# Performance work log

Hardware: AMD Instinct MI355X
Metric: run time of the kernel (lower is better)

## Reference

```python
import jax, jax.numpy as jnp
import numpy as np

N_NODES, N_EDGES, D_IN, D_OUT = 50000, 400000, 512, 512


def setup_inputs() -> dict:
    key = jax.random.key(0)
    k = jax.random.split(key, 7)
    s = 1.0 / np.sqrt(D_IN)
    return {
        "x": jax.random.normal(k[0], (N_NODES, D_IN), dtype=jnp.float32),
        "src": jax.random.randint(k[1], (N_EDGES,), 0, N_NODES),
        "dst": jax.random.randint(k[2], (N_EDGES,), 0, N_NODES),
        "W1": jax.random.uniform(k[3], (D_IN, D_OUT), jnp.float32, -s, s),
        "b1": jax.random.uniform(k[4], (D_OUT,), jnp.float32, -s, s),
        "W2": jax.random.uniform(k[5], (D_IN, D_OUT), jnp.float32, -s, s),
        "b2": jax.random.uniform(k[6], (D_OUT,), jnp.float32, -s, s),
    }


def reference(x, src, dst, W1, b1, W2, b2):
    n_nodes = x.shape[0]
    # gather src features along each edge, segment-sum into dst nodes
    msg_sum = jax.ops.segment_sum(x[src], dst, num_segments=n_nodes)      # [N, D_in]
    counts = jax.ops.segment_sum(jnp.ones_like(dst, dtype=x.dtype), dst,
                                 num_segments=n_nodes)                    # [N]
    mean = msg_sum / jnp.maximum(counts, 1.0)[:, None]                    # mailbox mean
    out = (x @ W1 + b1) + ((x - mean) @ W2 + b2)
    # DGL update_all leaves nodes with no incoming messages untouched
    return jnp.where((counts > 0)[:, None], out, x)
```

## Files before the change

kernel.cpp:

```cpp
#include <hip/hip_runtime.h>
#include <hip/hip_bf16.h>
#include <stdint.h>

typedef unsigned short u16;
typedef unsigned int   u32;

#define N_NODES 50000
#define N_EDGES 400000
#define DDIM    512

typedef __attribute__((ext_vector_type(8))) __bf16 bf16x8;
typedef __attribute__((ext_vector_type(4))) float  f32x4;

__device__ __forceinline__ float bflo(u32 d) { return __builtin_bit_cast(float, d << 16); }
__device__ __forceinline__ float bfhi(u32 d) { return __builtin_bit_cast(float, d & 0xffff0000u); }
__device__ __forceinline__ u16 f2bf(float f) {
    u32 u = __builtin_bit_cast(u32, f);
    u32 r = u + 0x7fffu + ((u >> 16) & 1u);
    return (u16)(r >> 16);
}
__device__ __forceinline__ u32 pack2(float a, float b) {
    return (u32)f2bf(a) | ((u32)f2bf(b) << 16);
}
__device__ __forceinline__ void gload_lds16(const void* g, void* l) {
    __builtin_amdgcn_global_load_lds(
        (const __attribute__((address_space(1))) void*)g,
        (__attribute__((address_space(3))) void*)l, 16, 0, 0);
}

__global__ void cvt_k(const float* __restrict__ x, u16* __restrict__ xb) {
    int i = blockIdx.x * 256 + threadIdx.x;
    const float4* p = (const float4*)(x + (size_t)i * 8);
    float4 a = p[0], b = p[1];
    uint4 o;
    o.x = pack2(a.x, a.y); o.y = pack2(a.z, a.w);
    o.z = pack2(b.x, b.y); o.w = pack2(b.z, b.w);
    ((uint4*)xb)[i] = o;
}

__global__ void hist_k(const int* __restrict__ dst, int* __restrict__ counts) {
    int e = blockIdx.x * 256 + threadIdx.x;
    if (e < N_EDGES) atomicAdd(&counts[dst[e]], 1);
}

#define NCHUNK 49
__global__ __launch_bounds__(1024) void scanA_k(const int* __restrict__ counts, int* __restrict__ csum) {
    __shared__ int ws[16];
    int t = threadIdx.x, b = blockIdx.x;
    int i = b * 1024 + t;
    int v = (i < N_NODES) ? counts[i] : 0;
    for (int d = 32; d; d >>= 1) v += __shfl_down(v, d);
    if ((t & 63) == 0) ws[t >> 6] = v;
    __syncthreads();
    if (t < 16) {
        int s = ws[t];
        for (int d = 8; d; d >>= 1) s += __shfl_down(s, d);
        if (t == 0) csum[b] = s;
    }
}
__global__ void scanB_k(int* __restrict__ csum) {
    int t = threadIdx.x;
    int v = (t < NCHUNK) ? csum[t] : 0;
    int s = v;
    for (int d = 1; d < 64; d <<= 1) { int u = __shfl_up(s, d); if (t >= d) s += u; }
    if (t < NCHUNK) csum[t] = s - v;
}
__global__ __launch_bounds__(1024) void scanC_k(const int* __restrict__ counts, const int* __restrict__ csum,
                                                int* __restrict__ offsets, int* __restrict__ cursor) {
    __shared__ int wsum[16];
    int t = threadIdx.x, b = blockIdx.x;
    int i = b * 1024 + t;
    int lane = t & 63, w = t >> 6;
    int v = (i < N_NODES) ? counts[i] : 0;
    int s = v;
    for (int d = 1; d < 64; d <<= 1) { int u = __shfl_up(s, d); if (lane >= d) s += u; }
    if (lane == 63) wsum[w] = s;
    __syncthreads();
    if (t < 16) {
        int ww = wsum[t], ss = ww;
        for (int d = 1; d < 16; d <<= 1) { int u = __shfl_up(ss, d); if (t >= d) ss += u; }
        wsum[t] = ss - ww;
    }
    __syncthreads();
    int excl = (s - v) + wsum[w] + csum[b];
    if (i < N_NODES) { offsets[i] = excl; cursor[i] = excl; }
}

__global__ void fill_k(const int* __restrict__ src, const int* __restrict__ dst,
                       int* __restrict__ cursor, int* __restrict__ esrc) {
    int e = blockIdx.x * 256 + threadIdx.x;
    if (e < N_EDGES) {
        int d = dst[e];
        int p = atomicAdd(&cursor[d], 1);
        esrc[p] = src[e];
    }
}

__global__ void prepw_k(const float* __restrict__ W1, const float* __restrict__ W2,
                        const float* __restrict__ b1, const float* __restrict__ b2,
                        u16* __restrict__ Wt12, u16* __restrict__ Wt2, float* __restrict__ b12) {
    int idx = blockIdx.x * 256 + threadIdx.x;
    int k = idx >> 9, n = idx & 511;
    float w1 = W1[idx], w2 = W2[idx];
    Wt12[n * 512 + k] = f2bf(w1 + w2);
    Wt2[n * 512 + k]  = f2bf(w2);
    if (idx < 512) b12[idx] = b1[idx] + b2[idx];
}

__device__ __forceinline__ void addrow(float* acc, uint4 v) {
    acc[0] += bflo(v.x); acc[1] += bfhi(v.x);
    acc[2] += bflo(v.y); acc[3] += bfhi(v.y);
    acc[4] += bflo(v.z); acc[5] += bfhi(v.z);
    acc[6] += bflo(v.w); acc[7] += bfhi(v.w);
}
__global__ __launch_bounds__(256) void agg_k(const u16* __restrict__ xb,
                                             const int* __restrict__ offsets,
                                             const int* __restrict__ counts,
                                             const int* __restrict__ esrc,
                                             u16* __restrict__ meanNeg) {
    int nid = blockIdx.x * 4 + (threadIdx.x >> 6);
    if (nid >= N_NODES) return;
    int lane = threadIdx.x & 63;
    int off = offsets[nid], deg = counts[nid];
    float acc[8] = {0, 0, 0, 0, 0, 0, 0, 0};
    int e = 0;
    for (; e + 3 < deg; e += 4) {
        int s0 = esrc[off + e], s1 = esrc[off + e + 1];
        int s2 = esrc[off + e + 2], s3 = esrc[off + e + 3];
        uint4 v0 = *(const uint4*)(xb + (size_t)s0 * DDIM + lane * 8);
        uint4 v1 = *(const uint4*)(xb + (size_t)s1 * DDIM + lane * 8);
        uint4 v2 = *(const uint4*)(xb + (size_t)s2 * DDIM + lane * 8);
        uint4 v3 = *(const uint4*)(xb + (size_t)s3 * DDIM + lane * 8);
        addrow(acc, v0); addrow(acc, v1); addrow(acc, v2); addrow(acc, v3);
    }
    for (; e < deg; e++) {
        int s0 = esrc[off + e];
        addrow(acc, *(const uint4*)(xb + (size_t)s0 * DDIM + lane * 8));
    }
    float scale = (deg > 0) ? (-1.0f / (float)deg) : 0.0f;
    uint4 o;
    o.x = pack2(acc[0] * scale, acc[1] * scale);
    o.y = pack2(acc[2] * scale, acc[3] * scale);
    o.z = pack2(acc[4] * scale, acc[5] * scale);
    o.w = pack2(acc[6] * scale, acc[7] * scale);
    *(uint4*)(meanNeg + (size_t)nid * DDIM + lane * 8) = o;
}

__global__ __launch_bounds__(256) void gemm_k(const u16* __restrict__ xb,
                                              const float* __restrict__ x,
                                              const u16* __restrict__ meanNeg,
                                              const u16* __restrict__ Wt12,
                                              const u16* __restrict__ Wt2,
                                              const float* __restrict__ b12,
                                              const int* __restrict__ counts,
                                              float* __restrict__ out) {
    __shared__ u16 As[128 * 32];
    __shared__ u16 Bs[128 * 32];
    const int m0 = blockIdx.x * 128;
    const int n0 = blockIdx.y * 128;
    const int tid = threadIdx.x;
    const int lane = tid & 63;
    const int wid  = tid >> 6;
    const int wm = wid >> 1, wn = wid & 1;
    const int quad = lane >> 4, lr = lane & 15;

    f32x4 acc[4][4] = {};

    const int skoff = (lane & 3) * 8;
    const int srsub = lane >> 2;
    int arow[2], brow[2];
    #pragma unroll
    for (int t = 0; t < 2; t++) {
        int r = wid * 32 + t * 16 + srsub;
        int ar = m0 + r; if (ar >= N_NODES) ar = N_NODES - 1;
        arow[t] = ar;
        brow[t] = n0 + r;
    }

    for (int pass = 0; pass < 2; pass++) {
        const u16* __restrict__ A = pass ? meanNeg : xb;
        const u16* __restrict__ B = pass ? Wt2 : Wt12;
        for (int k0 = 0; k0 < 512; k0 += 32) {
            #pragma unroll
            for (int t = 0; t < 2; t++) {
                int rblk = wid * 32 + t * 16;
                gload_lds16(A + (size_t)arow[t] * DDIM + k0 + skoff, &As[rblk * 32]);
                gload_lds16(B + (size_t)brow[t] * DDIM + k0 + skoff, &Bs[rblk * 32]);
            }
            __syncthreads();
            bf16x8 af[4], bfr[4];
            #pragma unroll
            for (int i = 0; i < 4; i++)
                af[i] = *(const bf16x8*)&As[(wm * 64 + i * 16 + lr) * 32 + quad * 8];
            #pragma unroll
            for (int j = 0; j < 4; j++)
                bfr[j] = *(const bf16x8*)&Bs[(wn * 64 + j * 16 + lr) * 32 + quad * 8];
            #pragma unroll
            for (int i = 0; i < 4; i++)
                #pragma unroll
                for (int j = 0; j < 4; j++)
                    acc[i][j] = __builtin_amdgcn_mfma_f32_16x16x32_bf16(af[i], bfr[j], acc[i][j], 0, 0, 0);
            __syncthreads();
        }
    }

    #pragma unroll
    for (int i = 0; i < 4; i++) {
        #pragma unroll
        for (int r = 0; r < 4; r++) {
            int grow = m0 + wm * 64 + i * 16 + quad * 4 + r;
            if (grow >= N_NODES) continue;
            int cnt = counts[grow];
            #pragma unroll
            for (int j = 0; j < 4; j++) {
                int gcol = n0 + wn * 64 + j * 16 + lr;
                float v;
                if (cnt > 0) v = acc[i][j][r] + b12[gcol];
                else         v = x[(size_t)grow * DDIM + gcol];
                out[(size_t)grow * DDIM + gcol] = v;
            }
        }
    }
}

extern "C" void kernel_launch(void* const* d_in, const int* in_sizes, int n_in,
                              void* d_out, int out_size, void* d_ws, size_t ws_size,
                              hipStream_t stream) {
    const float* x  = (const float*)d_in[0];
    const int* src  = (const int*)d_in[1];
    const int* dst  = (const int*)d_in[2];
    const float* W1 = (const float*)d_in[3];
    const float* b1 = (const float*)d_in[4];
    const float* W2 = (const float*)d_in[5];
    const float* b2 = (const float*)d_in[6];
    float* out = (float*)d_out;

    char* ws = (char*)d_ws;
    size_t o = 0;
    auto alloc = [&](size_t bytes) { char* p = ws + o; o += (bytes + 255) & ~(size_t)255; return p; };
    int* counts   = (int*)alloc((size_t)N_NODES * 4);
    int* offsets  = (int*)alloc((size_t)N_NODES * 4);
    int* cursor   = (int*)alloc((size_t)N_NODES * 4);
    int* csum     = (int*)alloc((size_t)NCHUNK * 4);
    int* esrc     = (int*)alloc((size_t)N_EDGES * 4);
    u16* Wt12     = (u16*)alloc((size_t)512 * 512 * 2);
    u16* Wt2      = (u16*)alloc((size_t)512 * 512 * 2);
    float* b12    = (float*)alloc((size_t)512 * 4);
    u16* xb       = (u16*)alloc((size_t)N_NODES * DDIM * 2);
    u16* meanNeg  = (u16*)alloc((size_t)N_NODES * DDIM * 2);
    (void)ws_size; (void)n_in; (void)in_sizes; (void)out_size;

    hipMemsetAsync(counts, 0, (size_t)N_NODES * 4, stream);
    cvt_k<<<(N_NODES * DDIM / 8) / 256, 256, 0, stream>>>(x, xb);
    hist_k<<<(N_EDGES + 255) / 256, 256, 0, stream>>>(dst, counts);
    scanA_k<<<NCHUNK, 1024, 0, stream>>>(counts, csum);
    scanB_k<<<1, 64, 0, stream>>>(csum);
    scanC_k<<<NCHUNK, 1024, 0, stream>>>(counts, csum, offsets, cursor);
    fill_k<<<(N_EDGES + 255) / 256, 256, 0, stream>>>(src, dst, cursor, esrc);
    prepw_k<<<(512 * 512) / 256, 256, 0, stream>>>(W1, W2, b1, b2, Wt12, Wt2, b12);
    agg_k<<<(N_NODES + 3) / 4, 256, 0, stream>>>(xb, offsets, counts, esrc, meanNeg);
    gemm_k<<<dim3((N_NODES + 127) / 128, DDIM / 128), 256, 0, stream>>>(
        xb, x, meanNeg, Wt12, Wt2, b12, counts, out);
}
```

Measured before the change: 433.9 us.

## Double GEMM K-tile, remap grid for L2 reuse, unroll aggregation by eight

The GEMM now stages 64-wide K tiles in LDS instead of 32, which halves the number of barrier pairs per pass. It also launches a 1D grid where the four N-tiles of one M-block are adjacent, so neighbouring blocks reuse the same A rows from L2. The aggregation kernel gains an 8-way unrolled gather loop to keep more row loads in flight. The trade-off is twice the LDS per block, which may reduce occupancy, plus higher register pressure in the aggregation kernel.

```diff
diff --git a/kernel.cpp b/kernel.cpp
--- a/kernel.cpp
+++ b/kernel.cpp
@@ -123,19 +123,36 @@
     int lane = threadIdx.x & 63;
     int off = offsets[nid], deg = counts[nid];
     float acc[8] = {0, 0, 0, 0, 0, 0, 0, 0};
+    const size_t lo = (size_t)lane * 8;
     int e = 0;
+    for (; e + 7 < deg; e += 8) {
+        int s0 = esrc[off + e],     s1 = esrc[off + e + 1];
+        int s2 = esrc[off + e + 2], s3 = esrc[off + e + 3];
+        int s4 = esrc[off + e + 4], s5 = esrc[off + e + 5];
+        int s6 = esrc[off + e + 6], s7 = esrc[off + e + 7];
+        uint4 v0 = *(const uint4*)(xb + (size_t)s0 * DDIM + lo);
+        uint4 v1 = *(const uint4*)(xb + (size_t)s1 * DDIM + lo);
+        uint4 v2 = *(const uint4*)(xb + (size_t)s2 * DDIM + lo);
+        uint4 v3 = *(const uint4*)(xb + (size_t)s3 * DDIM + lo);
+        uint4 v4 = *(const uint4*)(xb + (size_t)s4 * DDIM + lo);
+        uint4 v5 = *(const uint4*)(xb + (size_t)s5 * DDIM + lo);
+        uint4 v6 = *(const uint4*)(xb + (size_t)s6 * DDIM + lo);
+        uint4 v7 = *(const uint4*)(xb + (size_t)s7 * DDIM + lo);
+        addrow(acc, v0); addrow(acc, v1); addrow(acc, v2); addrow(acc, v3);
+        addrow(acc, v4); addrow(acc, v5); addrow(acc, v6); addrow(acc, v7);
+    }
     for (; e + 3 < deg; e += 4) {
-        int s0 = esrc[off + e], s1 = esrc[off + e + 1];
+        int s0 = esrc[off + e],     s1 = esrc[off + e + 1];
         int s2 = esrc[off + e + 2], s3 = esrc[off + e + 3];
-        uint4 v0 = *(const uint4*)(xb + (size_t)s0 * DDIM + lane * 8);
-        uint4 v1 = *(const uint4*)(xb + (size_t)s1 * DDIM + lane * 8);
-        uint4 v2 = *(const uint4*)(xb + (size_t)s2 * DDIM + lane * 8);
-        uint4 v3 = *(const uint4*)(xb + (size_t)s3 * DDIM + lane * 8);
+        uint4 v0 = *(const uint4*)(xb + (size_t)s0 * DDIM + lo);
+        uint4 v1 = *(const uint4*)(xb + (size_t)s1 * DDIM + lo);
+        uint4 v2 = *(const uint4*)(xb + (size_t)s2 * DDIM + lo);
+        uint4 v3 = *(const uint4*)(xb + (size_t)s3 * DDIM + lo);
         addrow(acc, v0); addrow(acc, v1); addrow(acc, v2); addrow(acc, v3);
     }
     for (; e < deg; e++) {
         int s0 = esrc[off + e];
-        addrow(acc, *(const uint4*)(xb + (size_t)s0 * DDIM + lane * 8));
+        addrow(acc, *(const uint4*)(xb + (size_t)s0 * DDIM + lo));
     }
     float scale = (deg > 0) ? (-1.0f / (float)deg) : 0.0f;
     uint4 o;
@@ -143,7 +160,7 @@
     o.y = pack2(acc[2] * scale, acc[3] * scale);
     o.z = pack2(acc[4] * scale, acc[5] * scale);
     o.w = pack2(acc[6] * scale, acc[7] * scale);
-    *(uint4*)(meanNeg + (size_t)nid * DDIM + lane * 8) = o;
+    *(uint4*)(meanNeg + (size_t)nid * DDIM + lo) = o;
 }
 
 __global__ __launch_bounds__(256) void gemm_k(const u16* __restrict__ xb,
@@ -154,10 +171,11 @@
                                               const float* __restrict__ b12,
                                               const int* __restrict__ counts,
                                               float* __restrict__ out) {
-    __shared__ u16 As[128 * 32];
-    __shared__ u16 Bs[128 * 32];
-    const int m0 = blockIdx.x * 128;
-    const int n0 = blockIdx.y * 128;
+    __shared__ u16 As[128 * 64];
+    __shared__ u16 Bs[128 * 64];
+    const int bid = blockIdx.x;
+    const int m0 = (bid >> 2) * 128;
+    const int n0 = (bid & 3) * 128;
     const int tid = threadIdx.x;
     const int lane = tid & 63;
     const int wid  = tid >> 6;
@@ -166,12 +184,11 @@
 
     f32x4 acc[4][4] = {};
 
-    const int skoff = (lane & 3) * 8;
-    const int srsub = lane >> 2;
-    int arow[2], brow[2];
+    const int kk = (lane & 7) * 8;
+    int arow[4], brow[4];
     #pragma unroll
-    for (int t = 0; t < 2; t++) {
-        int r = wid * 32 + t * 16 + srsub;
+    for (int t = 0; t < 4; t++) {
+        int r = wid * 32 + t * 8 + (lane >> 3);
         int ar = m0 + r; if (ar >= N_NODES) ar = N_NODES - 1;
         arow[t] = ar;
         brow[t] = n0 + r;
@@ -180,26 +197,29 @@
     for (int pass = 0; pass < 2; pass++) {
         const u16* __restrict__ A = pass ? meanNeg : xb;
         const u16* __restrict__ B = pass ? Wt2 : Wt12;
-        for (int k0 = 0; k0 < 512; k0 += 32) {
+        for (int k0 = 0; k0 < 512; k0 += 64) {
             #pragma unroll
-            for (int t = 0; t < 2; t++) {
-                int rblk = wid * 32 + t * 16;
-                gload_lds16(A + (size_t)arow[t] * DDIM + k0 + skoff, &As[rblk * 32]);
-                gload_lds16(B + (size_t)brow[t] * DDIM + k0 + skoff, &Bs[rblk * 32]);
+            for (int t = 0; t < 4; t++) {
+                int rblk = wid * 32 + t * 8;
+                gload_lds16(A + (size_t)arow[t] * DDIM + k0 + kk, &As[rblk * 64]);
+                gload_lds16(B + (size_t)brow[t] * DDIM + k0 + kk, &Bs[rblk * 64]);
             }
             __syncthreads();
-            bf16x8 af[4], bfr[4];
             #pragma unroll
-            for (int i = 0; i < 4; i++)
-                af[i] = *(const bf16x8*)&As[(wm * 64 + i * 16 + lr) * 32 + quad * 8];
-            #pragma unroll
-            for (int j = 0; j < 4; j++)
-                bfr[j] = *(const bf16x8*)&Bs[(wn * 64 + j * 16 + lr) * 32 + quad * 8];
-            #pragma unroll
-            for (int i = 0; i < 4; i++)
+            for (int ks = 0; ks < 2; ks++) {
+                bf16x8 af[4], bfr[4];
+                #pragma unroll
+                for (int i = 0; i < 4; i++)
+                    af[i] = *(const bf16x8*)&As[(wm * 64 + i * 16 + lr) * 64 + ks * 32 + quad * 8];
                 #pragma unroll
                 for (int j = 0; j < 4; j++)
-                    acc[i][j] = __builtin_amdgcn_mfma_f32_16x16x32_bf16(af[i], bfr[j], acc[i][j], 0, 0, 0);
+                    bfr[j] = *(const bf16x8*)&Bs[(wn * 64 + j * 16 + lr) * 64 + ks * 32 + quad * 8];
+                #pragma unroll
+                for (int i = 0; i < 4; i++)
+                    #pragma unroll
+                    for (int j = 0; j < 4; j++)
+                        acc[i][j] = __builtin_amdgcn_mfma_f32_16x16x32_bf16(af[i], bfr[j], acc[i][j], 0, 0, 0);
+            }
             __syncthreads();
         }
     }
@@ -259,6 +279,6 @@
     fill_k<<<(N_EDGES + 255) / 256, 256, 0, stream>>>(src, dst, cursor, esrc);
     prepw_k<<<(512 * 512) / 256, 256, 0, stream>>>(W1, W2, b1, b2, Wt12, Wt2, b12);
     agg_k<<<(N_NODES + 3) / 4, 256, 0, stream>>>(xb, offsets, counts, esrc, meanNeg);
-    gemm_k<<<dim3((N_NODES + 127) / 128, DDIM / 128), 256, 0, stream>>>(
+    gemm_k<<<391 * 4, 256, 0, stream>>>(
         xb, x, meanNeg, Wt12, Wt2, b12, counts, out);
 }
```

Result: no change. 435.4 us (+0.4%).
